# Performance work log

Measured on AMD Instinct MI355X. Metric: run time of the kernel, lower is better.

Reference implementation:

```python
import jax, jax.numpy as jnp
import numpy as np

ALPHA = 1.0

def setup_inputs() -> dict:
    key = jax.random.key(0)
    k1, k2 = jax.random.split(key)
    N, K, D = 524288, 256, 256
    context = jax.random.normal(k1, (N, D), dtype=jnp.float32)
    clusters = jax.random.normal(k2, (K, D), dtype=jnp.float32)
    return {"context": context, "clusters": clusters}

def reference(context, clusters):
    # Squared euclidean distance via the matmul trick: same math as
    # sum((x[:,None]-c)**2, -1) but avoids materializing (N,K,D).
    x2 = jnp.sum(context * context, axis=1, keepdims=True)          # (N,1)
    c2 = jnp.sum(clusters * clusters, axis=1)                       # (K,)
    xc = context @ clusters.T                                       # (N,K)
    distance = x2 + c2 - 2.0 * xc                                   # (N,K)
    q = 1.0 / (1.0 + distance / ALPHA)
    q = q ** ((ALPHA + 1.0) / 2.0)
    q = q / jnp.sum(q, axis=1, keepdims=True)                        # row-normalize
    return q
```

## Files before the change

kernel.cpp:

```cpp
#include <hip/hip_runtime.h>
#include <hip/hip_bf16.h>


#define DD 256
#define KC 256
#define BM 64

typedef __attribute__((ext_vector_type(4)))  float f32x4;
typedef __attribute__((ext_vector_type(16))) float f32x16;
typedef __attribute__((ext_vector_type(8)))  short bf16x8;
typedef __attribute__((ext_vector_type(4)))  short bf16x4;
typedef __attribute__((ext_vector_type(4)))  unsigned u32x4;

__device__ __forceinline__ short f2bf(float f) {
    union { float f; unsigned u; } v; v.f = f;
    unsigned r = (v.u + 0x7fffu + ((v.u >> 16) & 1u)) >> 16;
    return (short)r;
}

__device__ __forceinline__ float bf2f(short h) {
    return __builtin_bit_cast(float, ((unsigned)(unsigned short)h) << 16);
}

__device__ __forceinline__ unsigned cvtpk(float a, float b) {
    unsigned r;
    asm("v_cvt_pk_bf16_f32 %0, %1, %2" : "=v"(r) : "v"(a), "v"(b));
    return r;
}

__device__ __forceinline__ float frcp(float x) {
    return __builtin_amdgcn_rcpf(x);
}

template<int CTRL>
__device__ __forceinline__ float dpp_add(float v) {
    int iv = __builtin_bit_cast(int, v);
    int mv = __builtin_amdgcn_update_dpp(0, iv, CTRL, 0xf, 0xf, false);
    return v + __builtin_bit_cast(float, mv);
}
#define QUAD_SWAP1 0xB1

__device__ __forceinline__ f32x4 ld4(const float* p) { return *(const f32x4*)p; }

__global__ __launch_bounds__(64)
void prep_clusters(const float* __restrict__ clus, short* __restrict__ wsb) {
    const int c = blockIdx.x;
    const int t = threadIdx.x;
    f32x4 v = *(const f32x4*)(clus + c * DD + t * 4);
    bf16x4 o;
    o[0] = f2bf(-2.f * v[0]); o[1] = f2bf(-2.f * v[1]);
    o[2] = f2bf(-2.f * v[2]); o[3] = f2bf(-2.f * v[3]);

    const int j    = t >> 1;
    const int ks   = j >> 1;
    const int hi   = j & 1;
    const int half = t & 1;
    const int nj   = c >> 5;
    const int l31  = c & 31;
    *(bf16x4*)&wsb[(((nj * 17 + ks) * 64 + hi * 32 + l31) << 3) + half * 4] = o;

    float s = v[0]*v[0] + v[1]*v[1] + v[2]*v[2] + v[3]*v[3];
    s += __shfl_xor(s, 1);  s += __shfl_xor(s, 2);  s += __shfl_xor(s, 4);
    s += __shfl_xor(s, 8);  s += __shfl_xor(s, 16); s += __shfl_xor(s, 32);
    if (t == 0) {
        float e = 1.f + s;
        short h = f2bf(e);  float e1 = e - bf2f(h);
        short m = f2bf(e1); float e2 = e1 - bf2f(m);
        short l = f2bf(e2);
        const unsigned one = 0x3F80u;
        u32x4 a;
        a[0] = one | (one << 16);
        a[1] = one | ((unsigned)(unsigned short)h << 16);
        a[2] = (unsigned)(unsigned short)m | ((unsigned)(unsigned short)l << 16);
        a[3] = 0u;
        *(u32x4*)&wsb[((nj * 17 + 16) * 64 + l31) * 8] = a;
        u32x4 z = {0u, 0u, 0u, 0u};
        *(u32x4*)&wsb[((nj * 17 + 16) * 64 + 32 + l31) * 8] = z;
    }
}

__global__ __launch_bounds__(512, 6)
void cluster_q_main(const float* __restrict__ ctx,
                    const short* __restrict__ wsb,
                    float* __restrict__ out) {
    __shared__ short Af[34 * 64 * 8];
    __shared__ float x2p8[8][64];
    __shared__ float rowsum2[8][2][64];

    const int t    = threadIdx.x;
    const int lane = t & 63;
    const int w    = t >> 6;
    const int l31  = lane & 31;
    const int hi   = lane >> 5;
    const size_t row0 = (size_t)blockIdx.x * BM;

    {
        const int r0   = lane >> 1;
        const int half = lane & 1;
        f32x4 u[8];
#pragma unroll
        for (int m = 0; m < 2; ++m) {
            const float* src = ctx + (row0 + (size_t)(m * 32 + r0)) * DD
                             + w * 32 + half * 16;
#pragma unroll
            for (int i = 0; i < 4; ++i)
                u[m * 4 + i] = ld4(src + i * 4);
        }
#pragma unroll
        for (int m = 0; m < 2; ++m) {
            float xs = 0.f;
#pragma unroll
            for (int c = 0; c < 2; ++c) {
                f32x4 a0 = u[m * 4 + 2 * c], a1 = u[m * 4 + 2 * c + 1];
                u32x4 o;
                o[0] = cvtpk(a0[0], a0[1]);
                o[1] = cvtpk(a0[2], a0[3]);
                o[2] = cvtpk(a1[0], a1[1]);
                o[3] = cvtpk(a1[2], a1[3]);
                xs += a0[0]*a0[0] + a0[1]*a0[1] + a0[2]*a0[2] + a0[3]*a0[3]
                    + a1[0]*a1[0] + a1[1]*a1[1] + a1[2]*a1[2] + a1[3]*a1[3];
                const int j = w * 4 + half * 2 + c;
                *(u32x4*)&Af[(j * 64 + m * 32 + r0) * 8] = o;
            }
            xs = dpp_add<QUAD_SWAP1>(xs);
            if (half == 0) x2p8[w][m * 32 + r0] = xs;
        }
    }

    const short* bl = wsb + (size_t)(w * 17) * 512 + lane * 8;

    __syncthreads();

    if (w == 0) {
        float e = 0.f;
#pragma unroll
        for (int q = 0; q < 8; ++q) e += x2p8[q][lane];
        short h = f2bf(e);  float e1 = e - bf2f(h);
        short m = f2bf(e1); float e2 = e1 - bf2f(m);
        short l = f2bf(e2);
        const unsigned one = 0x3F80u;
        u32x4 o;
        o[0] = (unsigned)(unsigned short)h | ((unsigned)(unsigned short)m << 16);
        o[1] = (unsigned)(unsigned short)l | (one << 16);
        o[2] = one | (one << 16);
        o[3] = 0u;
        *(u32x4*)&Af[(32 * 64 + lane) * 8] = o;
        u32x4 z = {0u, 0u, 0u, 0u};
        *(u32x4*)&Af[(33 * 64 + lane) * 8] = z;
    }

    f32x16 acc0 = (f32x16)0.f, acc1 = (f32x16)0.f;

    bf16x8 bs[3];
    bs[0] = *(const bf16x8*)(bl + 0 * 512);
    bs[1] = *(const bf16x8*)(bl + 1 * 512);

    bf16x8 afA0 = *(const bf16x8*)&Af[((0 + hi) * 64 +  0 + l31) * 8];
    bf16x8 afA1 = *(const bf16x8*)&Af[((0 + hi) * 64 + 32 + l31) * 8];
    bf16x8 afB0, afB1;

#pragma unroll
    for (int ks = 0; ks < 16; ++ks) {
        const int cur = ks % 3;
        const bool even = (ks & 1) == 0;

        if (ks < 14)
            bs[(ks + 2) % 3] = *(const bf16x8*)(bl + (ks + 2) * 512);
        if (ks < 15) {
            const int jn = (ks + 1) * 2 + hi;
            bf16x8 v0 = *(const bf16x8*)&Af[(jn * 64 +  0 + l31) * 8];
            bf16x8 v1 = *(const bf16x8*)&Af[(jn * 64 + 32 + l31) * 8];
            if (even) { afB0 = v0; afB1 = v1; }
            else      { afA0 = v0; afA1 = v1; }
        }

        const bf16x8 a0 = even ? afA0 : afB0;
        const bf16x8 a1 = even ? afA1 : afB1;
        acc0 = __builtin_amdgcn_mfma_f32_32x32x16_bf16(bs[cur], a0, acc0, 0, 0, 0);
        acc1 = __builtin_amdgcn_mfma_f32_32x32x16_bf16(bs[cur], a1, acc1, 0, 0, 0);
    }

    bf16x8 bsa = *(const bf16x8*)(bl + 16 * 512);

    __syncthreads();

    {
        bf16x8 aa0 = *(const bf16x8*)&Af[((32 + hi) * 64 +  0 + l31) * 8];
        bf16x8 aa1 = *(const bf16x8*)&Af[((32 + hi) * 64 + 32 + l31) * 8];
        acc0 = __builtin_amdgcn_mfma_f32_32x32x16_bf16(bsa, aa0, acc0, 0, 0, 0);
        acc1 = __builtin_amdgcn_mfma_f32_32x32x16_bf16(bsa, aa1, acc1, 0, 0, 0);
    }

    float s0 = 0.f, s1 = 0.f;
#pragma unroll
    for (int r = 0; r < 16; ++r) {
        acc0[r] = frcp(acc0[r]); s0 += acc0[r];
        acc1[r] = frcp(acc1[r]); s1 += acc1[r];
    }
    rowsum2[w][hi][l31]      = s0;
    rowsum2[w][hi][32 + l31] = s1;
    __syncthreads();

    float t0 = 0.f, t1 = 0.f;
#pragma unroll
    for (int q = 0; q < 8; ++q) {
        t0 += rowsum2[q][0][l31]      + rowsum2[q][1][l31];
        t1 += rowsum2[q][0][32 + l31] + rowsum2[q][1][32 + l31];
    }
    const float inv0 = frcp(t0);
    const float inv1 = frcp(t1);

    float* op0 = out + (row0 + (size_t)l31) * KC        + w * 32 + 4 * hi;
    float* op1 = out + (row0 + (size_t)(32 + l31)) * KC + w * 32 + 4 * hi;
#pragma unroll
    for (int i = 0; i < 4; ++i) {
        f32x4 v0, v1;
#pragma unroll
        for (int j = 0; j < 4; ++j) {
            v0[j] = acc0[4 * i + j] * inv0;
            v1[j] = acc1[4 * i + j] * inv1;
        }
        *(f32x4*)(op0 + 8 * i) = v0;
        *(f32x4*)(op1 + 8 * i) = v1;
    }
}

extern "C" void kernel_launch(void* const* d_in, const int* in_sizes, int n_in,
                              void* d_out, int out_size, void* d_ws, size_t ws_size,
                              hipStream_t stream) {
    const float* ctx  = (const float*)d_in[0];
    const float* clus = (const float*)d_in[1];
    float* out = (float*)d_out;

    short* wsb = (short*)d_ws;

    const int nrows = in_sizes[0] / DD;
    const int grid  = nrows / BM;

    hipLaunchKernelGGL(prep_clusters, dim3(KC), dim3(64), 0, stream, clus, wsb);
    hipLaunchKernelGGL(cluster_q_main, dim3(grid), dim3(512), 0, stream,
                       ctx, wsb, out);
}
```

Measured before the change: 240.9 us.

## Process two row tiles per block, prefetching the next tile's context during MFMA

Each block now handles two 64-row tiles with double-buffered LDS. Global loads of the second tile's context are issued inside the first tile's MFMA loop to hide memory latency. The x² term moves out of the augmented MFMA column and is added in registers before the reciprocal, so one LDS augmentation write and one barrier go away. Launch bounds drop to 4 blocks per CU, and the extra live registers for the prefetched tile may reduce occupancy.

```diff
diff --git a/kernel.cpp b/kernel.cpp
--- a/kernel.cpp
+++ b/kernel.cpp
@@ -5,6 +5,7 @@
 #define DD 256
 #define KC 256
 #define BM 64
+#define NT 2
 
 typedef __attribute__((ext_vector_type(4)))  float f32x4;
 typedef __attribute__((ext_vector_type(16))) float f32x16;
@@ -67,24 +68,47 @@
         short h = f2bf(e);  float e1 = e - bf2f(h);
         short m = f2bf(e1); float e2 = e1 - bf2f(m);
         short l = f2bf(e2);
-        const unsigned one = 0x3F80u;
         u32x4 a;
-        a[0] = one | (one << 16);
-        a[1] = one | ((unsigned)(unsigned short)h << 16);
-        a[2] = (unsigned)(unsigned short)m | ((unsigned)(unsigned short)l << 16);
-        a[3] = 0u;
+        a[0] = (unsigned)(unsigned short)h | ((unsigned)(unsigned short)m << 16);
+        a[1] = (unsigned)(unsigned short)l;
+        a[2] = 0u; a[3] = 0u;
         *(u32x4*)&wsb[((nj * 17 + 16) * 64 + l31) * 8] = a;
         u32x4 z = {0u, 0u, 0u, 0u};
         *(u32x4*)&wsb[((nj * 17 + 16) * 64 + 32 + l31) * 8] = z;
     }
 }
 
-__global__ __launch_bounds__(512, 6)
+__device__ __forceinline__ void convert_tile(const f32x4* u, short* AfB,
+                                             float (*x2p)[64], int w, int lane) {
+    const int r0   = lane >> 1;
+    const int half = lane & 1;
+#pragma unroll
+    for (int m = 0; m < 2; ++m) {
+        float xs = 0.f;
+#pragma unroll
+        for (int c = 0; c < 2; ++c) {
+            f32x4 a0 = u[m * 4 + 2 * c], a1 = u[m * 4 + 2 * c + 1];
+            u32x4 o;
+            o[0] = cvtpk(a0[0], a0[1]);
+            o[1] = cvtpk(a0[2], a0[3]);
+            o[2] = cvtpk(a1[0], a1[1]);
+            o[3] = cvtpk(a1[2], a1[3]);
+            xs += a0[0]*a0[0] + a0[1]*a0[1] + a0[2]*a0[2] + a0[3]*a0[3]
+                + a1[0]*a1[0] + a1[1]*a1[1] + a1[2]*a1[2] + a1[3]*a1[3];
+            const int j = w * 4 + half * 2 + c;
+            *(u32x4*)&AfB[(j * 64 + m * 32 + r0) * 8] = o;
+        }
+        xs = dpp_add<QUAD_SWAP1>(xs);
+        if (half == 0) x2p[w][m * 32 + r0] = xs;
+    }
+}
+
+__global__ __launch_bounds__(512, 4)
 void cluster_q_main(const float* __restrict__ ctx,
                     const short* __restrict__ wsb,
                     float* __restrict__ out) {
-    __shared__ short Af[34 * 64 * 8];
-    __shared__ float x2p8[8][64];
+    __shared__ short Af[NT][32 * 64 * 8];
+    __shared__ float x2p8[NT][8][64];
     __shared__ float rowsum2[8][2][64];
 
     const int t    = threadIdx.x;
@@ -92,136 +116,121 @@
     const int w    = t >> 6;
     const int l31  = lane & 31;
     const int hi   = lane >> 5;
-    const size_t row0 = (size_t)blockIdx.x * BM;
-
-    {
-        const int r0   = lane >> 1;
-        const int half = lane & 1;
-        f32x4 u[8];
-#pragma unroll
-        for (int m = 0; m < 2; ++m) {
-            const float* src = ctx + (row0 + (size_t)(m * 32 + r0)) * DD
-                             + w * 32 + half * 16;
-#pragma unroll
-            for (int i = 0; i < 4; ++i)
-                u[m * 4 + i] = ld4(src + i * 4);
-        }
-#pragma unroll
-        for (int m = 0; m < 2; ++m) {
-            float xs = 0.f;
-#pragma unroll
-            for (int c = 0; c < 2; ++c) {
-                f32x4 a0 = u[m * 4 + 2 * c], a1 = u[m * 4 + 2 * c + 1];
-                u32x4 o;
-                o[0] = cvtpk(a0[0], a0[1]);
-                o[1] = cvtpk(a0[2], a0[3]);
-                o[2] = cvtpk(a1[0], a1[1]);
-                o[3] = cvtpk(a1[2], a1[3]);
-                xs += a0[0]*a0[0] + a0[1]*a0[1] + a0[2]*a0[2] + a0[3]*a0[3]
-                    + a1[0]*a1[0] + a1[1]*a1[1] + a1[2]*a1[2] + a1[3]*a1[3];
-                const int j = w * 4 + half * 2 + c;
-                *(u32x4*)&Af[(j * 64 + m * 32 + r0) * 8] = o;
+    const size_t row_blk = (size_t)blockIdx.x * (BM * NT);
+
+    const int r0   = lane >> 1;
+    const int half = lane & 1;
+    const float* src0 = ctx + (row_blk + (size_t)r0) * DD + w * 32 + half * 16;
+
+    f32x4 u[8];
+
+#pragma unroll
+    for (int jj = 0; jj < 8; ++jj)
+        u[jj] = ld4(src0 + (size_t)((jj >> 2) * 32) * DD + (jj & 3) * 4);
+    convert_tile(u, &Af[0][0], x2p8[0], w, lane);
+    __syncthreads();
+
+    const short* bl = wsb + (size_t)(w * 17) * 512 + lane * 8;
+
+    bf16x8 ctx_aug = (bf16x8)0;
+    if (hi == 0) {
+        ctx_aug[0] = (short)0x3F80; ctx_aug[1] = (short)0x3F80;
+        ctx_aug[2] = (short)0x3F80;
+    }
+
+#pragma unroll
+    for (int tile = 0; tile < NT; ++tile) {
+        const size_t trow = row_blk + (size_t)tile * BM;
+
+        float x2A = 0.f, x2B = 0.f;
+#pragma unroll
+        for (int q = 0; q < 8; ++q) {
+            x2A += x2p8[tile][q][l31];
+            x2B += x2p8[tile][q][32 + l31];
+        }
+
+        f32x16 acc0 = (f32x16)0.f, acc1 = (f32x16)0.f;
+
+        bf16x8 bs[3];
+        bs[0] = *(const bf16x8*)(bl + 0 * 512);
+        bs[1] = *(const bf16x8*)(bl + 1 * 512);
+        bf16x8 bsa = *(const bf16x8*)(bl + 16 * 512);
+
+        const short* AfC = &Af[tile][0];
+        bf16x8 afA0 = *(const bf16x8*)&AfC[((0 + hi) * 64 +  0 + l31) * 8];
+        bf16x8 afA1 = *(const bf16x8*)&AfC[((0 + hi) * 64 + 32 + l31) * 8];
+        bf16x8 afB0, afB1;
+
+#pragma unroll
+        for (int ks = 0; ks < 16; ++ks) {
+            const int cur = ks % 3;
+            const bool even = (ks & 1) == 0;
+
+            if (ks < 14)
+                bs[(ks + 2) % 3] = *(const bf16x8*)(bl + (ks + 2) * 512);
+            if (ks < 15) {
+                const int jn = (ks + 1) * 2 + hi;
+                bf16x8 v0 = *(const bf16x8*)&AfC[(jn * 64 +  0 + l31) * 8];
+                bf16x8 v1 = *(const bf16x8*)&AfC[(jn * 64 + 32 + l31) * 8];
+                if (even) { afB0 = v0; afB1 = v1; }
+                else      { afA0 = v0; afA1 = v1; }
             }
-            xs = dpp_add<QUAD_SWAP1>(xs);
-            if (half == 0) x2p8[w][m * 32 + r0] = xs;
-        }
-    }
-
-    const short* bl = wsb + (size_t)(w * 17) * 512 + lane * 8;
-
-    __syncthreads();
-
-    if (w == 0) {
-        float e = 0.f;
-#pragma unroll
-        for (int q = 0; q < 8; ++q) e += x2p8[q][lane];
-        short h = f2bf(e);  float e1 = e - bf2f(h);
-        short m = f2bf(e1); float e2 = e1 - bf2f(m);
-        short l = f2bf(e2);
-        const unsigned one = 0x3F80u;
-        u32x4 o;
-        o[0] = (unsigned)(unsigned short)h | ((unsigned)(unsigned short)m << 16);
-        o[1] = (unsigned)(unsigned short)l | (one << 16);
-        o[2] = one | (one << 16);
-        o[3] = 0u;
-        *(u32x4*)&Af[(32 * 64 + lane) * 8] = o;
-        u32x4 z = {0u, 0u, 0u, 0u};
-        *(u32x4*)&Af[(33 * 64 + lane) * 8] = z;
-    }
-
-    f32x16 acc0 = (f32x16)0.f, acc1 = (f32x16)0.f;
-
-    bf16x8 bs[3];
-    bs[0] = *(const bf16x8*)(bl + 0 * 512);
-    bs[1] = *(const bf16x8*)(bl + 1 * 512);
-
-    bf16x8 afA0 = *(const bf16x8*)&Af[((0 + hi) * 64 +  0 + l31) * 8];
-    bf16x8 afA1 = *(const bf16x8*)&Af[((0 + hi) * 64 + 32 + l31) * 8];
-    bf16x8 afB0, afB1;
-
-#pragma unroll
-    for (int ks = 0; ks < 16; ++ks) {
-        const int cur = ks % 3;
-        const bool even = (ks & 1) == 0;
-
-        if (ks < 14)
-            bs[(ks + 2) % 3] = *(const bf16x8*)(bl + (ks + 2) * 512);
-        if (ks < 15) {
-            const int jn = (ks + 1) * 2 + hi;
-            bf16x8 v0 = *(const bf16x8*)&Af[(jn * 64 +  0 + l31) * 8];
-            bf16x8 v1 = *(const bf16x8*)&Af[(jn * 64 + 32 + l31) * 8];
-            if (even) { afB0 = v0; afB1 = v1; }
-            else      { afA0 = v0; afA1 = v1; }
-        }
-
-        const bf16x8 a0 = even ? afA0 : afB0;
-        const bf16x8 a1 = even ? afA1 : afB1;
-        acc0 = __builtin_amdgcn_mfma_f32_32x32x16_bf16(bs[cur], a0, acc0, 0, 0, 0);
-        acc1 = __builtin_amdgcn_mfma_f32_32x32x16_bf16(bs[cur], a1, acc1, 0, 0, 0);
-    }
-
-    bf16x8 bsa = *(const bf16x8*)(bl + 16 * 512);
-
-    __syncthreads();
-
-    {
-        bf16x8 aa0 = *(const bf16x8*)&Af[((32 + hi) * 64 +  0 + l31) * 8];
-        bf16x8 aa1 = *(const bf16x8*)&Af[((32 + hi) * 64 + 32 + l31) * 8];
-        acc0 = __builtin_amdgcn_mfma_f32_32x32x16_bf16(bsa, aa0, acc0, 0, 0, 0);
-        acc1 = __builtin_amdgcn_mfma_f32_32x32x16_bf16(bsa, aa1, acc1, 0, 0, 0);
-    }
-
-    float s0 = 0.f, s1 = 0.f;
-#pragma unroll
-    for (int r = 0; r < 16; ++r) {
-        acc0[r] = frcp(acc0[r]); s0 += acc0[r];
-        acc1[r] = frcp(acc1[r]); s1 += acc1[r];
-    }
-    rowsum2[w][hi][l31]      = s0;
-    rowsum2[w][hi][32 + l31] = s1;
-    __syncthreads();
-
-    float t0 = 0.f, t1 = 0.f;
-#pragma unroll
-    for (int q = 0; q < 8; ++q) {
-        t0 += rowsum2[q][0][l31]      + rowsum2[q][1][l31];
-        t1 += rowsum2[q][0][32 + l31] + rowsum2[q][1][32 + l31];
-    }
-    const float inv0 = frcp(t0);
-    const float inv1 = frcp(t1);
-
-    float* op0 = out + (row0 + (size_t)l31) * KC        + w * 32 + 4 * hi;
-    float* op1 = out + (row0 + (size_t)(32 + l31)) * KC + w * 32 + 4 * hi;
-#pragma unroll
-    for (int i = 0; i < 4; ++i) {
-        f32x4 v0, v1;
-#pragma unroll
-        for (int j = 0; j < 4; ++j) {
-            v0[j] = acc0[4 * i + j] * inv0;
-            v1[j] = acc1[4 * i + j] * inv1;
-        }
-        *(f32x4*)(op0 + 8 * i) = v0;
-        *(f32x4*)(op1 + 8 * i) = v1;
+            if (tile + 1 < NT && (ks & 3) == 0) {
+                const int j0 = (ks >> 2) * 2;
+#pragma unroll
+                for (int jj = 0; jj < 2; ++jj) {
+                    const int jx = j0 + jj;
+                    u[jx] = ld4(src0 + (size_t)(BM + (jx >> 2) * 32) * DD
+                                     + (jx & 3) * 4);
+                }
+            }
+
+            const bf16x8 a0 = even ? afA0 : afB0;
+            const bf16x8 a1 = even ? afA1 : afB1;
+            acc0 = __builtin_amdgcn_mfma_f32_32x32x16_bf16(bs[cur], a0, acc0, 0, 0, 0);
+            acc1 = __builtin_amdgcn_mfma_f32_32x32x16_bf16(bs[cur], a1, acc1, 0, 0, 0);
+        }
+
+        acc0 = __builtin_amdgcn_mfma_f32_32x32x16_bf16(bsa, ctx_aug, acc0, 0, 0, 0);
+        acc1 = __builtin_amdgcn_mfma_f32_32x32x16_bf16(bsa, ctx_aug, acc1, 0, 0, 0);
+
+        float s0 = 0.f, s1 = 0.f;
+#pragma unroll
+        for (int r = 0; r < 16; ++r) {
+            acc0[r] = frcp(acc0[r] + x2A); s0 += acc0[r];
+            acc1[r] = frcp(acc1[r] + x2B); s1 += acc1[r];
+        }
+        rowsum2[w][hi][l31]      = s0;
+        rowsum2[w][hi][32 + l31] = s1;
+        __syncthreads();
+
+        float t0 = 0.f, t1 = 0.f;
+#pragma unroll
+        for (int q = 0; q < 8; ++q) {
+            t0 += rowsum2[q][0][l31]      + rowsum2[q][1][l31];
+            t1 += rowsum2[q][0][32 + l31] + rowsum2[q][1][32 + l31];
+        }
+        const float inv0 = frcp(t0);
+        const float inv1 = frcp(t1);
+
+        float* op0 = out + (trow + (size_t)l31) * KC        + w * 32 + 4 * hi;
+        float* op1 = out + (trow + (size_t)(32 + l31)) * KC + w * 32 + 4 * hi;
+#pragma unroll
+        for (int i = 0; i < 4; ++i) {
+            f32x4 v0, v1;
+#pragma unroll
+            for (int j = 0; j < 4; ++j) {
+                v0[j] = acc0[4 * i + j] * inv0;
+                v1[j] = acc1[4 * i + j] * inv1;
+            }
+            *(f32x4*)(op0 + 8 * i) = v0;
+            *(f32x4*)(op1 + 8 * i) = v1;
+        }
+
+        if (tile + 1 < NT) {
+            convert_tile(u, &Af[tile + 1][0], x2p8[tile + 1], w, lane);
+            __syncthreads();
+        }
     }
 }
 
@@ -235,7 +244,7 @@
     short* wsb = (short*)d_ws;
 
     const int nrows = in_sizes[0] / DD;
-    const int grid  = nrows / BM;
+    const int grid  = nrows / (BM * NT);
 
     hipLaunchKernelGGL(prep_clusters, dim3(KC), dim3(64), 0, stream, clus, wsb);
     hipLaunchKernelGGL(cluster_q_main, dim3(grid), dim3(512), 0, stream,
```

New measurement: 251.4 us. 4.3% more time.
